# Kernel tuning notes

Measured on AMD Instinct MI355X. Metric: run time of the kernel, lower is better.

Reference implementation:

```python
import jax, jax.numpy as jnp
import numpy as np

MIN_NORM = 1e-15
BALL_EPS = 1e-5  # projection margin for the Poincare ball


def _tanh(x):
    return jnp.tanh(jnp.clip(x, -15.0, 15.0))


def _artanh(x):
    return jnp.arctanh(jnp.clip(x, -1.0 + 1e-5, 1.0 - 1e-5))


def givens_rotations(r, x):
    # r, x: (N, d) with d even -> (N, d)
    g = r.reshape(r.shape[0], -1, 2)
    g = g / jnp.maximum(jnp.linalg.norm(g, axis=-1, keepdims=True), MIN_NORM)
    xp = x.reshape(x.shape[0], -1, 2)
    swap = jnp.concatenate([-xp[..., 1:], xp[..., :1]], axis=-1)
    return (g[..., :1] * xp + g[..., 1:] * swap).reshape(r.shape[0], -1)


def givens_reflection(r, x):
    g = r.reshape(r.shape[0], -1, 2)
    g = g / jnp.maximum(jnp.linalg.norm(g, axis=-1, keepdims=True), MIN_NORM)
    xp = x.reshape(x.shape[0], -1, 2)
    a = jnp.concatenate([xp[..., :1], -xp[..., 1:]], axis=-1)
    b = jnp.concatenate([xp[..., 1:], xp[..., :1]], axis=-1)
    return (g[..., :1] * a + g[..., 1:] * b).reshape(r.shape[0], -1)


def expmap0(u, c):
    sqrt_c = jnp.sqrt(c)
    u_norm = jnp.maximum(jnp.linalg.norm(u, axis=-1, keepdims=True), MIN_NORM)
    return _tanh(sqrt_c * u_norm) * u / (sqrt_c * u_norm)


def mobius_add(x, y, c):
    x2 = jnp.sum(x * x, -1, keepdims=True)
    y2 = jnp.sum(y * y, -1, keepdims=True)
    xy = jnp.sum(x * y, -1, keepdims=True)
    num = (1 + 2 * c * xy + c * y2) * x + (1 - c * x2) * y
    denom = 1 + 2 * c * xy + c * c * x2 * y2
    return num / jnp.maximum(denom, MIN_NORM)


def project(x, c):
    norm = jnp.maximum(jnp.linalg.norm(x, axis=-1, keepdims=True), MIN_NORM)
    maxnorm = (1.0 - BALL_EPS) / jnp.sqrt(c)
    return jnp.where(norm > maxnorm, x / norm * maxnorm, x)


def hyp_distance_multi_c_bmm(x, v, c):
    # x: (nc, cs, d) queries; v: (nc, ns, d) candidates; c: (nc, cs, 1) curvatures
    sqrt_c = jnp.sqrt(c)                                              # (nc, cs, 1)
    vnorm = jnp.linalg.norm(v, axis=-1, keepdims=True).transpose(0, 2, 1)  # (nc, 1, ns)
    xv = jnp.einsum('bcd,bnd->bcn', x, v) / vnorm                     # (nc, cs, ns)
    gamma = _tanh(sqrt_c * vnorm) / sqrt_c                            # (nc, cs, ns)
    x2 = jnp.sum(x * x, -1, keepdims=True)                            # (nc, cs, 1)
    c1 = 1 - 2 * c * gamma * xv + c * gamma ** 2
    c2 = 1 - c * x2
    num = jnp.sqrt(jnp.maximum(c1 ** 2 * x2 + c2 ** 2 * gamma ** 2 - 2 * c1 * c2 * gamma * xv, 0.0))
    denom = 1 - 2 * c * gamma * xv + c ** 2 * gamma ** 2 * x2
    dist = _artanh(sqrt_c * num / jnp.maximum(denom, MIN_NORM))
    return 2 * dist / sqrt_c                                          # (nc, cs, ns)


def setup_inputs() -> dict:
    key = jax.random.key(0)
    nc, cs, ns, d = 16, 1024, 1024, 512
    B = nc * cs
    ks = jax.random.split(key, 8)
    return {
        'head': jax.random.normal(ks[0], (B, d), jnp.float32),
        'head_bias': jax.random.normal(ks[1], (B, 1), jnp.float32),
        'rel': jax.random.normal(ks[2], (B, d), jnp.float32),
        'rel_diag': jax.random.normal(ks[3], (B, 2 * d), jnp.float32),
        'curvature': jax.random.normal(ks[4], (B, 1), jnp.float32),
        'context': jax.random.normal(ks[5], (B, d), jnp.float32),
        'scale': jnp.full((1,), 1.0 / np.sqrt(d), jnp.float32),
        'tail': jax.random.normal(ks[6], (nc * ns, d), jnp.float32),
        'tail_bias': jax.random.normal(ks[7], (nc * ns, 1), jnp.float32),
        'chunk_size': cs,
        'neg_sample_size': ns,
    }


def reference(head, head_bias, rel, rel_diag, curvature, context, scale, tail,
              tail_bias, chunk_size, neg_sample_size):
    num_chunk = head.shape[0] // chunk_size
    d = head.shape[-1]
    c = jax.nn.softplus(curvature)                                    # (B, 1)
    rot_mat, ref_mat = jnp.split(rel_diag, 2, axis=-1)
    rot_q = givens_rotations(rot_mat, head)[:, None, :]               # (B, 1, d)
    ref_q = givens_reflection(ref_mat, head)[:, None, :]              # (B, 1, d)
    cands = jnp.concatenate([ref_q, rot_q], axis=1)                   # (B, 2, d)
    att_w = jax.nn.softmax(
        jnp.sum(context[:, None, :] * cands * scale, -1, keepdims=True), axis=1)
    att_q = jnp.sum(att_w * cands, axis=1)                            # (B, d)
    lhs = expmap0(att_q, c)
    rel_h = expmap0(rel, c)
    res = project(mobius_add(lhs, rel_h, c), c)                       # (B, d)
    x = res.reshape(num_chunk, chunk_size, d)
    v = tail.reshape(num_chunk, neg_sample_size, d)
    c3 = c.reshape(num_chunk, chunk_size, 1)
    dist = hyp_distance_multi_c_bmm(x, v, c3)                         # (nc, cs, ns)
    score = (-dist ** 2
             + head_bias.reshape(num_chunk, chunk_size, 1)
             + tail_bias.reshape(num_chunk, 1, neg_sample_size))
    return score
```

## Files before the change

kernel.cpp:

```cpp
#include <hip/hip_runtime.h>
#include <math.h>

#define DEV static __device__ __forceinline__

constexpr float MIN_NORM = 1e-15f;
constexpr float BALL_EPS = 1e-5f;
constexpr int D = 512;

typedef float f32x4 __attribute__((ext_vector_type(4)));
typedef short short8v __attribute__((ext_vector_type(8)));
typedef unsigned short ushort8v __attribute__((ext_vector_type(8)));

DEV float rcpf_(float x) { return __builtin_amdgcn_rcpf(x); }
DEV float rsqf_(float x) { return __builtin_amdgcn_rsqf(x); }

DEV float tanh_over_a_pos(float a) {
    const float e = __expf(-2.0f * a);
    return (1.0f - e) * rcpf_((1.0f + e) * fmaxf(a, 1e-20f));
}

DEV unsigned short f2bf(float f) {
    unsigned int u = __float_as_uint(f);
    u = (u + 0x7FFFu + ((u >> 16) & 1u)) >> 16;
    return (unsigned short)u;
}
DEV float bf2f(unsigned short h) { return __uint_as_float(((unsigned int)h) << 16); }

DEV void write_packed_row(unsigned short* pack, size_t nrow, int row,
                          int lane, ushort8v hi, ushort8v lo)
{
    const int kb  = lane >> 2;
    const int cch = lane & 3;
    const int rx  = row & 7;
    unsigned short* dst = pack + ((size_t)kb * nrow + row) * 64;
    *(ushort8v*)(dst + ((cch ^ rx) * 8))       = hi;
    *(ushort8v*)(dst + (((cch + 4) ^ rx) * 8)) = lo;
}

__global__ __launch_bounds__(256, 2)
void prep_kernel(const float* __restrict__ head,
                 const float* __restrict__ rel,
                 const float* __restrict__ rel_diag,
                 const float* __restrict__ curvature,
                 const float* __restrict__ context,
                 const float* __restrict__ scale_p,
                 const float* __restrict__ tail,
                 unsigned short* __restrict__ packA,
                 unsigned short* __restrict__ packB,
                 float* __restrict__ row_x2,
                 float* __restrict__ row_c,
                 float* __restrict__ row_sc,
                 float* __restrict__ vnorm,
                 int B, int T)
{
    const int lane = threadIdx.x & 63;
    const int base = lane * 8;
    const int wid  = blockIdx.x * 4 + (threadIdx.x >> 6);
    const int r0   = wid * 2;

    if (r0 >= B) {
        const int tr = r0 - B;
        float v[2][8];
#pragma unroll
        for (int rr = 0; rr < 2; ++rr) {
            const size_t off = (size_t)(tr + rr) * D + base;
            *(float4*)&v[rr][0] = *(const float4*)(tail + off);
            *(float4*)&v[rr][4] = *(const float4*)(tail + off + 4);
        }
        __builtin_amdgcn_sched_barrier(0);
        float s[2] = {0.f, 0.f};
        ushort8v hi[2], lo[2];
#pragma unroll
        for (int rr = 0; rr < 2; ++rr)
#pragma unroll
            for (int e = 0; e < 8; ++e) {
                s[rr] += v[rr][e] * v[rr][e];
                const unsigned short hb_ = f2bf(v[rr][e]);
                hi[rr][e] = hb_;
                lo[rr][e] = f2bf(v[rr][e] - bf2f(hb_));
            }
        {
            const bool hsel = (lane & 1) != 0;
            const float z = hsel ? s[1] : s[0];
            const float g = hsel ? s[0] : s[1];
            float w = z + __shfl_xor(g, 1, 64);
#pragma unroll
            for (int o = 2; o <= 32; o <<= 1) w += __shfl_xor(w, o, 64);
            s[0] = __shfl(w, 0, 64);
            s[1] = __shfl(w, 1, 64);
        }
#pragma unroll
        for (int rr = 0; rr < 2; ++rr) {
            write_packed_row(packB, (size_t)T, tr + rr, lane, hi[rr], lo[rr]);
            if (lane == 0) vnorm[tr + rr] = sqrtf(s[rr]);
        }
        return;
    }

    float hv[2][8], rv[2][8], gv[2][8], fv[2][8], cxv[2][8];
    float cu[2];
#pragma unroll
    for (int rr = 0; rr < 2; ++rr) {
        const size_t roff = (size_t)(r0 + rr) * D + base;
        const size_t doff = (size_t)(r0 + rr) * 2 * D + base;
        *(float4*)&hv[rr][0]  = *(const float4*)(head + roff);
        *(float4*)&hv[rr][4]  = *(const float4*)(head + roff + 4);
        *(float4*)&rv[rr][0]  = *(const float4*)(rel + roff);
        *(float4*)&rv[rr][4]  = *(const float4*)(rel + roff + 4);
        *(float4*)&gv[rr][0]  = *(const float4*)(rel_diag + doff);
        *(float4*)&gv[rr][4]  = *(const float4*)(rel_diag + doff + 4);
        *(float4*)&fv[rr][0]  = *(const float4*)(rel_diag + doff + D);
        *(float4*)&fv[rr][4]  = *(const float4*)(rel_diag + doff + D + 4);
        *(float4*)&cxv[rr][0] = *(const float4*)(context + roff);
        *(float4*)&cxv[rr][4] = *(const float4*)(context + roff + 4);
        cu[rr] = curvature[r0 + rr];
    }
    const float sc = scale_p[0];
    __builtin_amdgcn_sched_barrier(0);

    float rq[2][8], rf[2][8];
#pragma unroll
    for (int rr = 0; rr < 2; ++rr)
#pragma unroll
        for (int p = 0; p < 4; ++p) {
            const float x0 = hv[rr][2*p], x1 = hv[rr][2*p+1];
            float g0 = gv[rr][2*p], g1 = gv[rr][2*p+1];
            const float gi = rsqf_(fmaxf(g0*g0 + g1*g1, 1e-30f));
            g0 *= gi; g1 *= gi;
            rq[rr][2*p]   = g0*x0 - g1*x1;
            rq[rr][2*p+1] = g0*x1 + g1*x0;
            float f0 = fv[rr][2*p], f1 = fv[rr][2*p+1];
            const float fi = rsqf_(fmaxf(f0*f0 + f1*f1, 1e-30f));
            f0 *= fi; f1 *= fi;
            rf[rr][2*p]   = f0*x0 + f1*x1;
            rf[rr][2*p+1] = f1*x0 - f0*x1;
        }

    float s[2][8];
#pragma unroll
    for (int rr = 0; rr < 2; ++rr) {
#pragma unroll
        for (int k = 0; k < 8; ++k) s[rr][k] = 0.f;
#pragma unroll
        for (int e = 0; e < 8; ++e) {
            s[rr][0] += cxv[rr][e]*rf[rr][e];   s[rr][1] += cxv[rr][e]*rq[rr][e];
            s[rr][2] += rv[rr][e]*rv[rr][e];    s[rr][3] += rf[rr][e]*rv[rr][e];
            s[rr][4] += rq[rr][e]*rv[rr][e];    s[rr][5] += rf[rr][e]*rf[rr][e];
            s[rr][6] += rq[rr][e]*rq[rr][e];    s[rr][7] += rf[rr][e]*rq[rr][e];
        }
    }

    float xf[16];
#pragma unroll
    for (int k = 0; k < 8; ++k) { xf[k] = s[0][k]; xf[8+k] = s[1][k]; }
#pragma unroll
    for (int rd = 0; rd < 4; ++rd) {
        const int o = 1 << rd;
        const int h = 8 >> rd;
        const bool hsel = (lane & o) != 0;
#pragma unroll
        for (int j = 0; j < 8; ++j) {
            if (j < h) {
                const float z = hsel ? xf[j + h] : xf[j];
                const float g = hsel ? xf[j] : xf[j + h];
                xf[j] = z + __shfl_xor(g, o, 64);
            }
        }
    }
    float vf = xf[0];
    vf += __shfl_xor(vf, 16, 64);
    vf += __shfl_xor(vf, 32, 64);
    float sall[16];
    {
        const int BR0 = 0, BR1 = 8, BR2 = 4, BR3 = 12, BR4_ = 2, BR5 = 10,
                  BR6 = 6, BR7 = 14, BR8 = 1, BR9 = 9, BR10 = 5, BR11 = 13,
                  BR12 = 3, BR13 = 11, BR14 = 7, BR15 = 15;
        sall[0]  = __shfl(vf, BR0, 64);   sall[1]  = __shfl(vf, BR1, 64);
        sall[2]  = __shfl(vf, BR2, 64);   sall[3]  = __shfl(vf, BR3, 64);
        sall[4]  = __shfl(vf, BR4_, 64);  sall[5]  = __shfl(vf, BR5, 64);
        sall[6]  = __shfl(vf, BR6, 64);   sall[7]  = __shfl(vf, BR7, 64);
        sall[8]  = __shfl(vf, BR8, 64);   sall[9]  = __shfl(vf, BR9, 64);
        sall[10] = __shfl(vf, BR10, 64);  sall[11] = __shfl(vf, BR11, 64);
        sall[12] = __shfl(vf, BR12, 64);  sall[13] = __shfl(vf, BR13, 64);
        sall[14] = __shfl(vf, BR14, 64);  sall[15] = __shfl(vf, BR15, 64);
    }
#pragma unroll
    for (int rr = 0; rr < 2; ++rr)
#pragma unroll
        for (int k = 0; k < 8; ++k) s[rr][k] = sall[rr * 8 + k];

    float pre[2][8], r2p[2];
    float cS[2], sqcS[2];
#pragma unroll
    for (int rr = 0; rr < 2; ++rr) {
        const float c  = fmaxf(cu[rr], 0.0f) + __logf(1.0f + __expf(-fabsf(cu[rr])));
        const float sqc = sqrtf(c);
        cS[rr] = c; sqcS[rr] = sqc;

        const float a0 = s[rr][0] * sc, a1 = s[rr][1] * sc;
        const float mx = fmaxf(a0, a1);
        const float e0 = __expf(a0 - mx), e1 = __expf(a1 - mx);
        const float w0 = e0 * rcpf_(e0 + e1);
        const float w1 = 1.0f - w0;

        const float att2    = fmaxf(w0*w0*s[rr][5] + 2.0f*w0*w1*s[rr][7] + w1*w1*s[rr][6], 0.0f);
        const float attdrel = w0*s[rr][3] + w1*s[rr][4];
        const float u_att = fmaxf(sqrtf(att2), MIN_NORM);
        const float u_rel = fmaxf(sqrtf(s[rr][2]), MIN_NORM);

        const float kl = tanh_over_a_pos(sqcS[rr] * u_att);
        const float kr = tanh_over_a_pos(sqcS[rr] * u_rel);

        const float x2 = kl*kl*att2;
        const float y2 = kr*kr*s[rr][2];
        const float xy = kl*kr*attdrel;

        const float Am  = 1.0f + 2.0f*c*xy + c*y2;
        const float Bm  = 1.0f - c*x2;
        const float inv_den = rcpf_(fmaxf(1.0f + 2.0f*c*xy + c*c*x2*y2, MIN_NORM));

        r2p[rr] = 0.f;
#pragma unroll
        for (int e = 0; e < 8; ++e) {
            const float attq = w0*rf[rr][e] + w1*rq[rr][e];
            pre[rr][e] = (Am*kl*attq + Bm*kr*rv[rr][e]) * inv_den;
            r2p[rr] += pre[rr][e]*pre[rr][e];
        }
    }
    {
        const bool hsel = (lane & 1) != 0;
        const float z = hsel ? r2p[1] : r2p[0];
        const float g = hsel ? r2p[0] : r2p[1];
        float w = z + __shfl_xor(g, 1, 64);
#pragma unroll
        for (int o = 2; o <= 32; o <<= 1) w += __shfl_xor(w, o, 64);
        r2p[0] = __shfl(w, 0, 64);
        r2p[1] = __shfl(w, 1, 64);
    }

#pragma unroll
    for (int rr = 0; rr < 2; ++rr) {
        const float nrm  = fmaxf(sqrtf(r2p[rr]), MIN_NORM);
        const float maxn = (1.0f - BALL_EPS) * rcpf_(sqcS[rr]);
        const float psc  = (nrm > maxn) ? (maxn * rcpf_(nrm)) : 1.0f;

        ushort8v hi, lo;
#pragma unroll
        for (int e = 0; e < 8; ++e) {
            const float o = pre[rr][e] * psc;
            const unsigned short hb_ = f2bf(o);
            hi[e] = hb_;
            lo[e] = f2bf(o - bf2f(hb_));
        }
        write_packed_row(packA, (size_t)B, r0 + rr, lane, hi, lo);

        if (lane == 0) {
            row_x2[r0 + rr] = r2p[rr] * psc * psc;
            row_c[r0 + rr]  = cS[rr];
            row_sc[r0 + rr] = sqcS[rr];
        }
    }
}

__global__ __launch_bounds__(512, 2)
void score_kernel(const unsigned short* __restrict__ packA,
                  const unsigned short* __restrict__ packB,
                  const float* __restrict__ vnorm,
                  const float* __restrict__ row_x2,
                  const float* __restrict__ row_c,
                  const float* __restrict__ row_sc,
                  const float* __restrict__ head_bias,
                  const float* __restrict__ tail_bias,
                  float* __restrict__ out,
                  int cs, int ns, int nrowA, int nrowB)
{
    extern __shared__ __align__(16) char smem[];

    const int orig = blockIdx.x;
    const int wg = (orig & 7) * 32 + (orig >> 3);
    const int bz = wg >> 4;
    const int by = (wg >> 2) & 3;
    const int bx = wg & 3;
    const int m0 = by * 256;
    const int n0 = bx * 256;

    const int tid  = threadIdx.x;
    const int lane = tid & 63;
    const int w    = tid >> 6;
    const int wr   = w >> 2, wn = w & 3;
    const int lrow = lane & 15, lg = lane >> 4;

    f32x4 acc[8][4];
#pragma unroll
    for (int i = 0; i < 8; ++i)
#pragma unroll
        for (int j = 0; j < 4; ++j) acc[i][j] = f32x4{0.f, 0.f, 0.f, 0.f};

    const int xr = (lg ^ (lrow & 7)) * 16;
    const int baseA = (wr * 128 + lrow) * 128 + xr;
    const int baseB = 32768 + (wn * 64 + lrow) * 128 + xr;

    const int s16 = (tid & 255) * 16;
    const int shi = tid >> 8;

    const char* gA = (const char*)packA + (size_t)(bz * cs + m0) * 128;
    const char* gB = (const char*)packB + (size_t)(bz * ns + n0) * 128;
    const size_t strA = (size_t)nrowA * 128;
    const size_t strB = (size_t)nrowB * 128;

#define GLL(srcp, dstp)                                                        \
    __builtin_amdgcn_global_load_lds(                                          \
        (const __attribute__((address_space(1))) unsigned int*)(srcp),         \
        (__attribute__((address_space(3))) unsigned int*)(dstp), 16, 0, 0)

#define STAGE(dstbase, srcpanel, off0, sstr)                                   \
    do { const int o_ = (off0) + s16 + shi * (sstr);                           \
         GLL((srcpanel) + o_, (dstbase) + o_); } while (0)

#define STAGE_ALL(dstslot, srcA, srcB)                                         \
    do {                                                                       \
        STAGE(dstslot, srcA, 0, 4096);      STAGE(dstslot, srcA, 16384, 4096); \
        STAGE(dstslot, srcA, 8192, 4096);   STAGE(dstslot, srcA, 24576, 4096); \
        STAGE((dstslot)+32768, srcB, 0, 8192);                                 \
        STAGE((dstslot)+32768, srcB, 16384, 8192);                             \
        STAGE((dstslot)+32768, srcB, 4096, 8192);                              \
        STAGE((dstslot)+32768, srcB, 20480, 8192);                             \
    } while (0)

#define RD(p, off) (*(const short8v*)((p) + (off)))
#define MFMA_(A_, B_, C_) __builtin_amdgcn_mfma_f32_16x16x32_bf16(A_, B_, C_, 0, 0, 0)

#define QUAD(MOFF, NOFF)                                                       \
    do {                                                                       \
        _Pragma("unroll") for (int mm = 0; mm < 4; ++mm)                       \
        _Pragma("unroll") for (int nn = 0; nn < 2; ++nn)                       \
            acc[(MOFF)+mm][(NOFF)+nn] = MFMA_(ah[mm], bh[(NOFF)+nn], acc[(MOFF)+mm][(NOFF)+nn]); \
        _Pragma("unroll") for (int mm = 0; mm < 4; ++mm)                       \
        _Pragma("unroll") for (int nn = 0; nn < 2; ++nn)                       \
            acc[(MOFF)+mm][(NOFF)+nn] = MFMA_(ah[mm], bl[(NOFF)+nn], acc[(MOFF)+mm][(NOFF)+nn]); \
        _Pragma("unroll") for (int mm = 0; mm < 4; ++mm)                       \
        _Pragma("unroll") for (int nn = 0; nn < 2; ++nn)                       \
            acc[(MOFF)+mm][(NOFF)+nn] = MFMA_(al[mm], bh[(NOFF)+nn], acc[(MOFF)+mm][(NOFF)+nn]); \
    } while (0)

#define BAR()   __builtin_amdgcn_s_barrier()
#define VM0()   asm volatile("s_waitcnt vmcnt(0)" ::: "memory")

    STAGE_ALL(smem, gA, gB);
    VM0();
    BAR();

    short8v ah[4], al[4], bh[4], bl[4];

#pragma unroll 1
    for (int t = 0; t < 16; ++t) {
        char* cur = smem + (t & 1) * 65536;
        char* oth = smem + ((t + 1) & 1) * 65536;

        if (t < 15)
            STAGE_ALL(oth, gA + (size_t)(t + 1) * strA, gB + (size_t)(t + 1) * strB);

#pragma unroll
        for (int m = 0; m < 4; ++m) {
            ah[m] = RD(cur, baseA + m * 2048);
            al[m] = RD(cur, (baseA ^ 64) + m * 2048);
        }
#pragma unroll
        for (int n = 0; n < 2; ++n) {
            bh[n] = RD(cur, baseB + n * 2048);
            bl[n] = RD(cur, (baseB ^ 64) + n * 2048);
        }
        QUAD(0, 0);
#pragma unroll
        for (int n = 2; n < 4; ++n) {
            bh[n] = RD(cur, baseB + n * 2048);
            bl[n] = RD(cur, (baseB ^ 64) + n * 2048);
        }
        QUAD(0, 2);
#pragma unroll
        for (int m = 0; m < 4; ++m) {
            ah[m] = RD(cur, baseA + 8192 + m * 2048);
            al[m] = RD(cur, (baseA ^ 64) + 8192 + m * 2048);
        }
        QUAD(4, 2);
        QUAD(4, 0);

        VM0();
        BAR();
    }

    const int nbase = n0 + wn * 64 + lrow;
    float rvn[4], vnv[4], tb[4];
#pragma unroll
    for (int j = 0; j < 4; ++j) {
        const int gn = bz * ns + nbase + j * 16;
        const float vn = vnorm[gn];
        vnv[j] = vn;
        rvn[j] = 1.0f / vn;
        tb[j]  = tail_bias[gn];
    }
#pragma unroll
    for (int i = 0; i < 8; ++i) {
#pragma unroll
        for (int q = 0; q < 4; ++q) {
            const int gm = bz * cs + m0 + wr * 128 + i * 16 + lg * 4 + q;
            const float x2  = row_x2[gm];
            const float cc  = row_c[gm];
            const float scq = row_sc[gm];
            const float hb  = head_bias[gm];
            const float rscq = 1.0f / scq;
            float* orow = out + (size_t)gm * ns + nbase;
#pragma unroll
            for (int j = 0; j < 4; ++j) {
                const float xv = acc[i][j][q] * rvn[j];
                float xx = fminf(scq * vnv[j], 15.0f);
                const float ey = __expf(2.0f * xx);
                const float g  = (1.0f - 2.0f / (ey + 1.0f)) * rscq;
                const float c1 = 1.0f - 2.0f*cc*g*xv + cc*g*g;
                const float c2 = 1.0f - cc*x2;
                const float num = sqrtf(fmaxf(c1*c1*x2 + c2*c2*g*g - 2.0f*c1*c2*g*xv, 0.0f));
                const float den = fmaxf(1.0f - 2.0f*cc*g*xv + cc*cc*g*g*x2, MIN_NORM);
                float tt = scq * num * __builtin_amdgcn_rcpf(den);
                tt = fminf(tt, 1.0f - 1e-5f);
                const float ath = 0.5f * __logf((1.0f + tt) * __builtin_amdgcn_rcpf(1.0f - tt));
                const float dist = 2.0f * rscq * ath;
                orow[j * 16] = -dist * dist + hb + tb[j];
            }
        }
    }
#undef GLL
#undef STAGE
#undef STAGE_ALL
#undef RD
#undef MFMA_
#undef QUAD
#undef BAR
#undef VM0
}

extern "C" void kernel_launch(void* const* d_in, const int* in_sizes, int n_in,
                              void* d_out, int out_size, void* d_ws, size_t ws_size,
                              hipStream_t stream)
{
    const float* head      = (const float*)d_in[0];
    const float* head_bias = (const float*)d_in[1];
    const float* rel       = (const float*)d_in[2];
    const float* rel_diag  = (const float*)d_in[3];
    const float* curvature = (const float*)d_in[4];
    const float* context   = (const float*)d_in[5];
    const float* scale     = (const float*)d_in[6];
    const float* tail      = (const float*)d_in[7];
    const float* tail_bias = (const float*)d_in[8];

    const int B  = in_sizes[1];
    const int T  = in_sizes[8];
    const int ns = out_size / B;
    const int nc = T / ns;
    const int cs = B / nc;

    unsigned short* packA = (unsigned short*)d_ws;
    unsigned short* packB = packA + (size_t)16 * B * 64;
    float* row_x2 = (float*)(packB + (size_t)16 * T * 64);
    float* row_c  = row_x2 + B;
    float* row_sc = row_c + B;
    float* vnormb = row_sc + B;

    prep_kernel<<<(B + T) / 8, 256, 0, stream>>>(head, rel, rel_diag, curvature,
                                                 context, scale, tail, packA, packB,
                                                 row_x2, row_c, row_sc, vnormb, B, T);

    (void)hipFuncSetAttribute((const void*)score_kernel,
                              hipFuncAttributeMaxDynamicSharedMemorySize, 131072);
    const int nblk = (ns / 256) * (cs / 256) * nc;
    score_kernel<<<nblk, 512, 131072, stream>>>(packA, packB, vnormb, row_x2, row_c,
                                                row_sc, head_bias, tail_bias,
                                                (float*)d_out, cs, ns, B, T);
}
```

Before: 126.2 us.

## Use 256x128 tiles with triple-buffered LDS pipeline in score kernel

Shrinks the N tile of the score GEMM from 256 to 128, doubling the block count, and replaces double-buffered staging with a three-slot ring that prefetches two K-steps ahead. Waiting on vmcnt(6) lets one tile's loads stay in flight while the current tile is computed, instead of draining all loads each iteration. LDS per block rises to 144KB and launch bounds drop to one block per CU, so it trades occupancy and more A-panel rereads for deeper overlap and better load balance.

```diff
diff --git a/kernel.cpp b/kernel.cpp
--- a/kernel.cpp
+++ b/kernel.cpp
@@ -172,17 +172,14 @@
     vf += __shfl_xor(vf, 32, 64);
     float sall[16];
     {
-        const int BR0 = 0, BR1 = 8, BR2 = 4, BR3 = 12, BR4_ = 2, BR5 = 10,
-                  BR6 = 6, BR7 = 14, BR8 = 1, BR9 = 9, BR10 = 5, BR11 = 13,
-                  BR12 = 3, BR13 = 11, BR14 = 7, BR15 = 15;
-        sall[0]  = __shfl(vf, BR0, 64);   sall[1]  = __shfl(vf, BR1, 64);
-        sall[2]  = __shfl(vf, BR2, 64);   sall[3]  = __shfl(vf, BR3, 64);
-        sall[4]  = __shfl(vf, BR4_, 64);  sall[5]  = __shfl(vf, BR5, 64);
-        sall[6]  = __shfl(vf, BR6, 64);   sall[7]  = __shfl(vf, BR7, 64);
-        sall[8]  = __shfl(vf, BR8, 64);   sall[9]  = __shfl(vf, BR9, 64);
-        sall[10] = __shfl(vf, BR10, 64);  sall[11] = __shfl(vf, BR11, 64);
-        sall[12] = __shfl(vf, BR12, 64);  sall[13] = __shfl(vf, BR13, 64);
-        sall[14] = __shfl(vf, BR14, 64);  sall[15] = __shfl(vf, BR15, 64);
+        sall[0]  = __shfl(vf, 0, 64);   sall[1]  = __shfl(vf, 8, 64);
+        sall[2]  = __shfl(vf, 4, 64);   sall[3]  = __shfl(vf, 12, 64);
+        sall[4]  = __shfl(vf, 2, 64);   sall[5]  = __shfl(vf, 10, 64);
+        sall[6]  = __shfl(vf, 6, 64);   sall[7]  = __shfl(vf, 14, 64);
+        sall[8]  = __shfl(vf, 1, 64);   sall[9]  = __shfl(vf, 9, 64);
+        sall[10] = __shfl(vf, 5, 64);   sall[11] = __shfl(vf, 13, 64);
+        sall[12] = __shfl(vf, 3, 64);   sall[13] = __shfl(vf, 11, 64);
+        sall[14] = __shfl(vf, 7, 64);   sall[15] = __shfl(vf, 15, 64);
     }
 #pragma unroll
     for (int rr = 0; rr < 2; ++rr)
@@ -262,7 +259,7 @@
     }
 }
 
-__global__ __launch_bounds__(512, 2)
+__global__ __launch_bounds__(512, 1)
 void score_kernel(const unsigned short* __restrict__ packA,
                   const unsigned short* __restrict__ packB,
                   const float* __restrict__ vnorm,
@@ -277,12 +274,12 @@
     extern __shared__ __align__(16) char smem[];
 
     const int orig = blockIdx.x;
-    const int wg = (orig & 7) * 32 + (orig >> 3);
-    const int bz = wg >> 4;
-    const int by = (wg >> 2) & 3;
-    const int bx = wg & 3;
+    const int wg = (orig & 7) * 64 + (orig >> 3);
+    const int bz = wg >> 5;
+    const int by = (wg >> 3) & 3;
+    const int bx = wg & 7;
     const int m0 = by * 256;
-    const int n0 = bx * 256;
+    const int n0 = bx * 128;
 
     const int tid  = threadIdx.x;
     const int lane = tid & 63;
@@ -290,109 +287,96 @@
     const int wr   = w >> 2, wn = w & 3;
     const int lrow = lane & 15, lg = lane >> 4;
 
-    f32x4 acc[8][4];
+    f32x4 acc[8][2];
 #pragma unroll
     for (int i = 0; i < 8; ++i)
 #pragma unroll
-        for (int j = 0; j < 4; ++j) acc[i][j] = f32x4{0.f, 0.f, 0.f, 0.f};
+        for (int j = 0; j < 2; ++j) acc[i][j] = f32x4{0.f, 0.f, 0.f, 0.f};
 
     const int xr = (lg ^ (lrow & 7)) * 16;
     const int baseA = (wr * 128 + lrow) * 128 + xr;
-    const int baseB = 32768 + (wn * 64 + lrow) * 128 + xr;
-
-    const int s16 = (tid & 255) * 16;
-    const int shi = tid >> 8;
+    const int baseB = 32768 + (wn * 32 + lrow) * 128 + xr;
 
     const char* gA = (const char*)packA + (size_t)(bz * cs + m0) * 128;
     const char* gB = (const char*)packB + (size_t)(bz * ns + n0) * 128;
     const size_t strA = (size_t)nrowA * 128;
     const size_t strB = (size_t)nrowB * 128;
+    const int t16 = tid * 16;
 
 #define GLL(srcp, dstp)                                                        \
     __builtin_amdgcn_global_load_lds(                                          \
         (const __attribute__((address_space(1))) unsigned int*)(srcp),         \
         (__attribute__((address_space(3))) unsigned int*)(dstp), 16, 0, 0)
 
-#define STAGE(dstbase, srcpanel, off0, sstr)                                   \
-    do { const int o_ = (off0) + s16 + shi * (sstr);                           \
-         GLL((srcpanel) + o_, (dstbase) + o_); } while (0)
-
-#define STAGE_ALL(dstslot, srcA, srcB)                                         \
+#define STAGE_TILE(slotbase, srcA, srcB)                                       \
     do {                                                                       \
-        STAGE(dstslot, srcA, 0, 4096);      STAGE(dstslot, srcA, 16384, 4096); \
-        STAGE(dstslot, srcA, 8192, 4096);   STAGE(dstslot, srcA, 24576, 4096); \
-        STAGE((dstslot)+32768, srcB, 0, 8192);                                 \
-        STAGE((dstslot)+32768, srcB, 16384, 8192);                             \
-        STAGE((dstslot)+32768, srcB, 4096, 8192);                              \
-        STAGE((dstslot)+32768, srcB, 20480, 8192);                             \
+        GLL((srcA) + t16,         (slotbase) + t16);                           \
+        GLL((srcA) + 8192 + t16,  (slotbase) + 8192 + t16);                    \
+        GLL((srcA) + 16384 + t16, (slotbase) + 16384 + t16);                   \
+        GLL((srcA) + 24576 + t16, (slotbase) + 24576 + t16);                   \
+        GLL((srcB) + t16,         (slotbase) + 32768 + t16);                   \
+        GLL((srcB) + 8192 + t16,  (slotbase) + 40960 + t16);                   \
     } while (0)
 
 #define RD(p, off) (*(const short8v*)((p) + (off)))
 #define MFMA_(A_, B_, C_) __builtin_amdgcn_mfma_f32_16x16x32_bf16(A_, B_, C_, 0, 0, 0)
-
-#define QUAD(MOFF, NOFF)                                                       \
+#define BAR()   __builtin_amdgcn_s_barrier()
+
+#define HALF(MOFF)                                                             \
     do {                                                                       \
         _Pragma("unroll") for (int mm = 0; mm < 4; ++mm)                       \
         _Pragma("unroll") for (int nn = 0; nn < 2; ++nn)                       \
-            acc[(MOFF)+mm][(NOFF)+nn] = MFMA_(ah[mm], bh[(NOFF)+nn], acc[(MOFF)+mm][(NOFF)+nn]); \
+            acc[(MOFF)+mm][nn] = MFMA_(ah[mm], bh[nn], acc[(MOFF)+mm][nn]);    \
         _Pragma("unroll") for (int mm = 0; mm < 4; ++mm)                       \
         _Pragma("unroll") for (int nn = 0; nn < 2; ++nn)                       \
-            acc[(MOFF)+mm][(NOFF)+nn] = MFMA_(ah[mm], bl[(NOFF)+nn], acc[(MOFF)+mm][(NOFF)+nn]); \
+            acc[(MOFF)+mm][nn] = MFMA_(ah[mm], bl[nn], acc[(MOFF)+mm][nn]);    \
         _Pragma("unroll") for (int mm = 0; mm < 4; ++mm)                       \
         _Pragma("unroll") for (int nn = 0; nn < 2; ++nn)                       \
-            acc[(MOFF)+mm][(NOFF)+nn] = MFMA_(al[mm], bh[(NOFF)+nn], acc[(MOFF)+mm][(NOFF)+nn]); \
+            acc[(MOFF)+mm][nn] = MFMA_(al[mm], bh[nn], acc[(MOFF)+mm][nn]);    \
     } while (0)
 
-#define BAR()   __builtin_amdgcn_s_barrier()
-#define VM0()   asm volatile("s_waitcnt vmcnt(0)" ::: "memory")
-
-    STAGE_ALL(smem, gA, gB);
-    VM0();
+    STAGE_TILE(smem, gA, gB);
+    STAGE_TILE(smem + 49152, gA + strA, gB + strB);
+    asm volatile("s_waitcnt vmcnt(6)" ::: "memory");
     BAR();
 
-    short8v ah[4], al[4], bh[4], bl[4];
+    short8v ah[4], al[4], bh[2], bl[2];
 
 #pragma unroll 1
     for (int t = 0; t < 16; ++t) {
-        char* cur = smem + (t & 1) * 65536;
-        char* oth = smem + ((t + 1) & 1) * 65536;
-
-        if (t < 15)
-            STAGE_ALL(oth, gA + (size_t)(t + 1) * strA, gB + (size_t)(t + 1) * strB);
-
+        char* cur = smem + (t % 3) * 49152;
+
+        if (t < 14)
+            STAGE_TILE(smem + ((t + 2) % 3) * 49152,
+                       gA + (size_t)(t + 2) * strA, gB + (size_t)(t + 2) * strB);
+
+#pragma unroll
+        for (int n = 0; n < 2; ++n) {
+            bh[n] = RD(cur, baseB + n * 2048);
+            bl[n] = RD(cur, (baseB ^ 64) + n * 2048);
+        }
 #pragma unroll
         for (int m = 0; m < 4; ++m) {
             ah[m] = RD(cur, baseA + m * 2048);
             al[m] = RD(cur, (baseA ^ 64) + m * 2048);
         }
-#pragma unroll
-        for (int n = 0; n < 2; ++n) {
-            bh[n] = RD(cur, baseB + n * 2048);
-            bl[n] = RD(cur, (baseB ^ 64) + n * 2048);
-        }
-        QUAD(0, 0);
-#pragma unroll
-        for (int n = 2; n < 4; ++n) {
-            bh[n] = RD(cur, baseB + n * 2048);
-            bl[n] = RD(cur, (baseB ^ 64) + n * 2048);
-        }
-        QUAD(0, 2);
+        HALF(0);
 #pragma unroll
         for (int m = 0; m < 4; ++m) {
             ah[m] = RD(cur, baseA + 8192 + m * 2048);
             al[m] = RD(cur, (baseA ^ 64) + 8192 + m * 2048);
         }
-        QUAD(4, 2);
-        QUAD(4, 0);
-
-        VM0();
+        HALF(4);
+
+        if (t < 14)       asm volatile("s_waitcnt vmcnt(6)" ::: "memory");
+        else if (t == 14) asm volatile("s_waitcnt vmcnt(0)" ::: "memory");
         BAR();
     }
 
-    const int nbase = n0 + wn * 64 + lrow;
-    float rvn[4], vnv[4], tb[4];
-#pragma unroll
-    for (int j = 0; j < 4; ++j) {
+    const int nbase = n0 + wn * 32 + lrow;
+    float rvn[2], vnv[2], tb[2];
+#pragma unroll
+    for (int j = 0; j < 2; ++j) {
         const int gn = bz * ns + nbase + j * 16;
         const float vn = vnorm[gn];
         vnv[j] = vn;
@@ -411,7 +395,7 @@
             const float rscq = 1.0f / scq;
             float* orow = out + (size_t)gm * ns + nbase;
 #pragma unroll
-            for (int j = 0; j < 4; ++j) {
+            for (int j = 0; j < 2; ++j) {
                 const float xv = acc[i][j][q] * rvn[j];
                 float xx = fminf(scq * vnv[j], 15.0f);
                 const float ey = __expf(2.0f * xx);
@@ -429,13 +413,11 @@
         }
     }
 #undef GLL
-#undef STAGE
-#undef STAGE_ALL
+#undef STAGE_TILE
 #undef RD
 #undef MFMA_
-#undef QUAD
+#undef HALF
 #undef BAR
-#undef VM0
 }
 
 extern "C" void kernel_launch(void* const* d_in, const int* in_sizes, int n_in,
@@ -470,9 +452,9 @@
                                                  row_x2, row_c, row_sc, vnormb, B, T);
 
     (void)hipFuncSetAttribute((const void*)score_kernel,
-                              hipFuncAttributeMaxDynamicSharedMemorySize, 131072);
-    const int nblk = (ns / 256) * (cs / 256) * nc;
-    score_kernel<<<nblk, 512, 131072, stream>>>(packA, packB, vnormb, row_x2, row_c,
+                              hipFuncAttributeMaxDynamicSharedMemorySize, 147456);
+    const int nblk = (ns / 128) * (cs / 256) * nc;
+    score_kernel<<<nblk, 512, 147456, stream>>>(packA, packB, vnormb, row_x2, row_c,
                                                 row_sc, head_bias, tail_bias,
                                                 (float*)d_out, cs, ns, B, T);
 }
```

Result: slower. 136.7 us (+8.3%).
